# Kernel tuning notes

Hardware: AMD Instinct MI355X
Metric: run time of the kernel (lower is better)

Reference implementation:

```python
import jax, jax.numpy as jnp
import numpy as np

N_NODES = 50000
N_EDGES = 640000
DIMS = [128, 256, 128]


def setup_inputs() -> dict:
    key = jax.random.key(0)
    ks = jax.random.split(key, 8)
    x = jax.random.normal(ks[0], (N_NODES, DIMS[0]), dtype=jnp.float32)
    src = jax.random.randint(ks[1], (N_EDGES,), 0, N_NODES)
    dst = jax.random.randint(ks[2], (N_EDGES,), 0, N_NODES)
    # ensure no pre-existing self loops so add_remaining_self_loops == append all loops
    dst = jnp.where(dst == src, (dst + 1) % N_NODES, dst)
    edge_index = jnp.stack([src, dst]).astype(jnp.int64)
    # SAGEConv lin_l weights (root_weight=False -> only neighbor linear), Kaiming-ish init
    def lin(k, fan_in, fan_out):
        s = 1.0 / np.sqrt(fan_in)
        kw, kb = jax.random.split(k)
        W = jax.random.uniform(kw, (fan_out, fan_in), minval=-s, maxval=s, dtype=jnp.float32)
        b = jax.random.uniform(kb, (fan_out,), minval=-s, maxval=s, dtype=jnp.float32)
        return W, b
    W1, b1 = lin(ks[3], DIMS[0], DIMS[1])
    W2, b2 = lin(ks[4], DIMS[1], DIMS[2])
    logit_scale = jnp.asarray(np.log(1.0 / 0.07), dtype=jnp.float32)
    return {"x": x, "edge_index": edge_index, "W1": W1, "b1": b1,
            "W2": W2, "b2": b2, "logit_scale": logit_scale}


def reference(x, edge_index, W1, b1, W2, b2, logit_scale):
    N = x.shape[0]
    loops = jnp.arange(N, dtype=edge_index.dtype)
    src = jnp.concatenate([edge_index[0], loops])  # add_remaining_self_loops
    dst = jnp.concatenate([edge_index[1], loops])
    deg = jax.ops.segment_sum(jnp.ones_like(dst, dtype=x.dtype), dst, num_segments=N)
    inv_deg = 1.0 / deg  # deg >= 1 thanks to self loops

    def sage_conv(y, W, b):
        # mean aggregation of source features at destination, then linear
        agg = jax.ops.segment_sum(y[src], dst, num_segments=N) * inv_deg[:, None]
        return agg @ W.T + b

    y = jax.nn.relu(sage_conv(x, W1, b1))
    y = sage_conv(y, W2, b2)
    # F.normalize(p=2, dim=-1, eps=1e-12)
    nrm = jnp.maximum(jnp.linalg.norm(y, axis=-1, keepdims=True), 1e-12)
    y = y / nrm
    return y * jnp.exp(logit_scale)
```

## Files before the change

kernel.cpp:

```cpp
#include <hip/hip_runtime.h>
#include <hip/hip_bf16.h>

#define N_NODES 50000
#define NPAD 50048
#define ZROW N_NODES
#define D0 128
#define D1 256
#define D2 128
#define N4 1600000
#define NB4 1601536
#define CAP 128

typedef __attribute__((ext_vector_type(8))) short short8;
typedef __attribute__((ext_vector_type(8))) unsigned short ushort8;
typedef __attribute__((ext_vector_type(4))) float f32x4;

static __device__ __forceinline__ unsigned short f2bf(float f) {
    __hip_bfloat16 h = __float2bfloat16(f);
    return *(unsigned short*)&h;
}
static __device__ __forceinline__ float bf2f(unsigned short u) {
    return __uint_as_float(((unsigned int)u) << 16);
}

__global__ __launch_bounds__(256) void k_prep(const float* __restrict__ x,
                                              unsigned short* __restrict__ x_bf,
                                              int* __restrict__ cursor,
                                              const float* __restrict__ W1,
                                              const float* __restrict__ W2,
                                              unsigned short* __restrict__ W1p,
                                              unsigned short* __restrict__ W2p,
                                              const int* __restrict__ ei32,
                                              int* __restrict__ flag) {
    int idx = blockIdx.x * 256 + threadIdx.x;
    if (idx < N4) {
        float4 v = ((const float4*)x)[idx];
        ushort4 u;
        u.x = f2bf(v.x); u.y = f2bf(v.y); u.z = f2bf(v.z); u.w = f2bf(v.w);
        ((ushort4*)x_bf)[idx] = u;
    } else if (idx < NB4) {
        ushort4 z = {0, 0, 0, 0};
        ((ushort4*)x_bf)[idx] = z;
    }
    if (idx < N_NODES) cursor[idx] = 0;
    if (idx < 2 * D0 * D1) {
        if (idx < D0 * D1) {
            int j = idx & 7, lane = (idx >> 3) & 63, tile = idx >> 9;
            int ct = tile & 15, kt = tile >> 4;
            int k = kt * 32 + (lane >> 4) * 8 + j;
            int n = ct * 16 + (lane & 15);
            W1p[idx] = f2bf(W1[n * D0 + k]);
        } else {
            int i2 = idx - D0 * D1;
            int j = i2 & 7, lane = (i2 >> 3) & 63, tile = i2 >> 9;
            int ct = tile & 7, kt = tile >> 3;
            int k = kt * 32 + (lane >> 4) * 8 + j;
            int n = ct * 16 + (lane & 15);
            W2p[i2] = f2bf(W2[n * D1 + k]);
        }
    }
    if (blockIdx.x == gridDim.x - 1 && threadIdx.x < 64) {
        int lane = threadIdx.x;
        int nz = 0;
#pragma unroll
        for (int k = 0; k < 16; k++) nz += (ei32[2 * (lane * 16 + k) + 1] != 0);
#pragma unroll
        for (int off = 32; off > 0; off >>= 1) nz += __shfl_down(nz, off, 64);
        if (lane == 0) *flag = (nz == 0) ? 1 : 0;
    }
}

__global__ __launch_bounds__(256) void k_bucket(const int* __restrict__ ei,
                                                int* __restrict__ cursor,
                                                int* __restrict__ csr, int E,
                                                const int* __restrict__ flag) {
    int i = blockIdx.x * 256 + threadIdx.x;
    if (2 * i >= E) return;
    int is64 = *flag;
    int s0, d0, s1, d1;
    if (is64) {
        int4 sp = ((const int4*)ei)[i];
        int4 dp = ((const int4*)(ei + 2 * (size_t)E))[i];
        s0 = sp.x; s1 = sp.z; d0 = dp.x; d1 = dp.z;
    } else {
        int2 sp = ((const int2*)ei)[i];
        int2 dp = ((const int2*)(ei + (size_t)E))[i];
        s0 = sp.x; s1 = sp.y; d0 = dp.x; d1 = dp.y;
    }
    int p0 = atomicAdd(&cursor[d0], 1);
    if (p0 < CAP) csr[(size_t)d0 * CAP + p0] = s0;
    if (2 * i + 1 < E) {
        int p1 = atomicAdd(&cursor[d1], 1);
        if (p1 < CAP) csr[(size_t)d1 * CAP + p1] = s1;
    }
}

#define H_LD 260
__global__ __launch_bounds__(256, 4) void k_gmlp(const unsigned short* __restrict__ x_bf,
                                                 const int* __restrict__ csr,
                                                 const int* __restrict__ cursor,
                                                 const unsigned short* __restrict__ W1p,
                                                 const float* __restrict__ b1,
                                                 const unsigned short* __restrict__ W2p,
                                                 unsigned short* __restrict__ t_bf) {
    __shared__ unsigned short sbuf[4][16 * H_LD];
    int tid = threadIdx.x;
    int n0 = blockIdx.x * 64;
    int w = tid >> 6, lane = tid & 63;
    int m = lane & 15, q = lane >> 4;
    unsigned short* wbuf = sbuf[w];

    {
        int h = lane & 15;
        int sub = lane >> 4;
#pragma unroll
        for (int r = 0; r < 4; r++) {
            int lrow = r * 4 + sub;
            int node = n0 + w * 16 + lrow;
            unsigned short* lp = wbuf + lrow * H_LD + h * 8;
            if (node < N_NODES) {
                float a0[8], a1[8];
                ushort8 u = *(const ushort8*)(x_bf + (size_t)node * 128 + h * 8);
#pragma unroll
                for (int t = 0; t < 8; t++) { a0[t] = bf2f(u[t]); a1[t] = 0.f; }
                int dg = cursor[node]; if (dg > CAP) dg = CAP;
                const int* cp = csr + (size_t)node * CAP;
                int jn = (dg + 7) & ~7;
                for (int j = 0; j < jn; j += 8) {
                    int idx[8];
#pragma unroll
                    for (int u8 = 0; u8 < 8; u8++) {
                        int jj = j + u8;
                        idx[u8] = (jj < dg) ? cp[jj] : ZROW;
                    }
                    ushort8 rr[8];
#pragma unroll
                    for (int u8 = 0; u8 < 8; u8++)
                        rr[u8] = *(const ushort8*)(x_bf + (size_t)idx[u8] * 128 + h * 8);
#pragma unroll
                    for (int t = 0; t < 8; t++) {
                        a0[t] += bf2f(rr[0][t]) + bf2f(rr[2][t]) + bf2f(rr[4][t]) + bf2f(rr[6][t]);
                        a1[t] += bf2f(rr[1][t]) + bf2f(rr[3][t]) + bf2f(rr[5][t]) + bf2f(rr[7][t]);
                    }
                }
                float invd = 1.0f / (float)(dg + 1);
                ushort8 o;
#pragma unroll
                for (int t = 0; t < 8; t++) o[t] = f2bf((a0[t] + a1[t]) * invd);
                *(ushort8*)lp = o;
            } else {
                ushort8 z = {0, 0, 0, 0, 0, 0, 0, 0};
                *(ushort8*)lp = z;
            }
        }
    }

    {
        short8 af[4];
        const unsigned short* arow = wbuf + m * H_LD + q * 8;
#pragma unroll
        for (int kt = 0; kt < 4; kt++) af[kt] = *(const short8*)(arow + kt * 32);
#pragma unroll
        for (int ct = 0; ct < 16; ct++) {
            f32x4 acc = {0.f, 0.f, 0.f, 0.f};
#pragma unroll
            for (int kt = 0; kt < 4; kt++) {
                short8 bf = *(const short8*)(W1p + (((kt * 16 + ct) * 64 + lane) << 3));
                acc = __builtin_amdgcn_mfma_f32_16x16x32_bf16(af[kt], bf, acc, 0, 0, 0);
            }
            int c = ct * 16 + m;
            float bias = b1[c];
#pragma unroll
            for (int r = 0; r < 4; r++) {
                float v = fmaxf(acc[r] + bias, 0.0f);
                wbuf[(q * 4 + r) * H_LD + c] = f2bf(v);
            }
        }
    }

    {
        short8 hf[8];
        const unsigned short* hrow = wbuf + m * H_LD + q * 8;
#pragma unroll
        for (int kt = 0; kt < 8; kt++) hf[kt] = *(const short8*)(hrow + kt * 32);
#pragma unroll
        for (int ct = 0; ct < 8; ct++) {
            f32x4 acc = {0.f, 0.f, 0.f, 0.f};
#pragma unroll
            for (int kt = 0; kt < 8; kt++) {
                short8 bf = *(const short8*)(W2p + (((kt * 8 + ct) * 64 + lane) << 3));
                acc = __builtin_amdgcn_mfma_f32_16x16x32_bf16(hf[kt], bf, acc, 0, 0, 0);
            }
            int c = ct * 16 + m;
#pragma unroll
            for (int r = 0; r < 4; r++) {
                int node = n0 + w * 16 + q * 4 + r;
                t_bf[(size_t)node * 128 + c] = (node < N_NODES) ? f2bf(acc[r]) : (unsigned short)0;
            }
        }
    }
}

__global__ __launch_bounds__(256) void k_gather_final(const unsigned short* __restrict__ t,
                                                      const int* __restrict__ csr,
                                                      const int* __restrict__ cursor,
                                                      const float* __restrict__ b2,
                                                      const float* __restrict__ ls,
                                                      float* __restrict__ out) {
    int tid = threadIdx.x;
    int h = tid & 15;
    int node = blockIdx.x * 16 + (tid >> 4);

    float a0[8], a1[8];
    ushort8 u = *(const ushort8*)(t + (size_t)node * 128 + h * 8);
#pragma unroll
    for (int k = 0; k < 8; k++) { a0[k] = bf2f(u[k]); a1[k] = 0.f; }
    int dg = cursor[node]; if (dg > CAP) dg = CAP;
    const int* cp = csr + (size_t)node * CAP;
    int jn = (dg + 7) & ~7;
    for (int j = 0; j < jn; j += 8) {
        int idx[8];
#pragma unroll
        for (int u8 = 0; u8 < 8; u8++) {
            int jj = j + u8;
            idx[u8] = (jj < dg) ? cp[jj] : ZROW;
        }
        ushort8 rr[8];
#pragma unroll
        for (int u8 = 0; u8 < 8; u8++)
            rr[u8] = *(const ushort8*)(t + (size_t)idx[u8] * 128 + h * 8);
#pragma unroll
        for (int k = 0; k < 8; k++) {
            a0[k] += bf2f(rr[0][k]) + bf2f(rr[2][k]) + bf2f(rr[4][k]) + bf2f(rr[6][k]);
            a1[k] += bf2f(rr[1][k]) + bf2f(rr[3][k]) + bf2f(rr[5][k]) + bf2f(rr[7][k]);
        }
    }
    float invd = 1.0f / (float)(dg + 1);
    float4 bb0 = ((const float4*)b2)[h * 2];
    float4 bb1 = ((const float4*)b2)[h * 2 + 1];
    float v[8];
    v[0] = (a0[0] + a1[0]) * invd + bb0.x;
    v[1] = (a0[1] + a1[1]) * invd + bb0.y;
    v[2] = (a0[2] + a1[2]) * invd + bb0.z;
    v[3] = (a0[3] + a1[3]) * invd + bb0.w;
    v[4] = (a0[4] + a1[4]) * invd + bb1.x;
    v[5] = (a0[5] + a1[5]) * invd + bb1.y;
    v[6] = (a0[6] + a1[6]) * invd + bb1.z;
    v[7] = (a0[7] + a1[7]) * invd + bb1.w;

    float s = 0.f;
#pragma unroll
    for (int k = 0; k < 8; k++) s += v[k] * v[k];
#pragma unroll
    for (int msk = 8; msk > 0; msk >>= 1) s += __shfl_xor(s, msk, 64);
    float nrm = fmaxf(sqrtf(s), 1e-12f);
    float scale = expf(ls[0]) / nrm;
    float4 o0, o1;
    o0.x = v[0] * scale; o0.y = v[1] * scale; o0.z = v[2] * scale; o0.w = v[3] * scale;
    o1.x = v[4] * scale; o1.y = v[5] * scale; o1.z = v[6] * scale; o1.w = v[7] * scale;
    float* op = out + (size_t)node * 128 + h * 8;
    *(float4*)(op + 0) = o0;
    *(float4*)(op + 4) = o1;
}

extern "C" void kernel_launch(void* const* d_in, const int* in_sizes, int n_in,
                              void* d_out, int out_size, void* d_ws, size_t ws_size,
                              hipStream_t stream) {
    const float* x  = (const float*)d_in[0];
    const int*   ei = (const int*)d_in[1];
    const float* W1 = (const float*)d_in[2];
    const float* b1 = (const float*)d_in[3];
    const float* W2 = (const float*)d_in[4];
    const float* b2 = (const float*)d_in[5];
    const float* ls = (const float*)d_in[6];
    float* out = (float*)d_out;

    const int E = in_sizes[1] / 2;

    char* ws = (char*)d_ws;
    size_t off = 0;
    auto alloc = [&](size_t bytes) {
        size_t o = off;
        off = (off + bytes + 255) & ~(size_t)255;
        return o;
    };
    int*            flag   = (int*)(ws + alloc(256));
    int*            cursor = (int*)(ws + alloc((size_t)N_NODES * 4));
    int*            csr    = (int*)(ws + alloc((size_t)N_NODES * CAP * 4));
    unsigned short* W1p    = (unsigned short*)(ws + alloc((size_t)D0 * D1 * 2));
    unsigned short* W2p    = (unsigned short*)(ws + alloc((size_t)D1 * D2 * 2));
    unsigned short* x_bf   = (unsigned short*)(ws + alloc((size_t)NPAD * D0 * 2));
    unsigned short* t_bf   = (unsigned short*)(ws + alloc((size_t)NPAD * D2 * 2));

    k_prep<<<(NB4 + 255) / 256, 256, 0, stream>>>(x, x_bf, cursor, W1, W2, W1p, W2p, ei, flag);
    k_bucket<<<(E / 2 + 255) / 256, 256, 0, stream>>>(ei, cursor, csr, E, flag);
    k_gmlp<<<NPAD / 64, 256, 0, stream>>>(x_bf, csr, cursor, W1p, b1, W2p, t_bf);
    k_gather_final<<<N_NODES / 16, 256, 0, stream>>>(t_bf, csr, cursor, b2, ls, out);
}
```

Baseline: 212.6 us.

## Fuse edge bucketing into prep kernel and restructure gather-MLP work split

Merges the edge bucketing into the prep kernel. Each block re-detects the int64 index layout itself and a memset zeroes the cursor, which removes one kernel launch and the flag round trip. k_gmlp now handles 16 nodes per block: all 256 threads share the gather, then the waves split the MLP output columns, and occupancy is raised to 6. Both gathers batch the first 16 neighbor indices with vector loads so more loads are in flight. In exchange, the weight fragments are re-read by four times as many blocks, and the bucketing atomics now run in the same kernel as the conversion work.

New measurement: 200.4 us. 5.7% less time.

```diff
diff --git a/kernel.cpp b/kernel.cpp
--- a/kernel.cpp
+++ b/kernel.cpp
@@ -25,14 +25,46 @@
 
 __global__ __launch_bounds__(256) void k_prep(const float* __restrict__ x,
                                               unsigned short* __restrict__ x_bf,
-                                              int* __restrict__ cursor,
                                               const float* __restrict__ W1,
                                               const float* __restrict__ W2,
                                               unsigned short* __restrict__ W1p,
                                               unsigned short* __restrict__ W2p,
-                                              const int* __restrict__ ei32,
-                                              int* __restrict__ flag) {
+                                              const int* __restrict__ ei,
+                                              int* __restrict__ cursor,
+                                              int* __restrict__ csr, int E) {
+    __shared__ int s_is64;
+    if (threadIdx.x < 64) {
+        int lane = threadIdx.x;
+        int nz = 0;
+#pragma unroll
+        for (int k = 0; k < 16; k++) nz += (ei[2 * (lane * 16 + k) + 1] != 0);
+#pragma unroll
+        for (int off = 32; off > 0; off >>= 1) nz += __shfl_down(nz, off, 64);
+        if (lane == 0) s_is64 = (nz == 0) ? 1 : 0;
+    }
+    __syncthreads();
     int idx = blockIdx.x * 256 + threadIdx.x;
+
+    if (2 * idx < E) {
+        int is64 = s_is64;
+        int es0, ed0, es1, ed1;
+        if (is64) {
+            int4 sp = ((const int4*)ei)[idx];
+            int4 dp = ((const int4*)(ei + 2 * (size_t)E))[idx];
+            es0 = sp.x; es1 = sp.z; ed0 = dp.x; ed1 = dp.z;
+        } else {
+            int2 sp = ((const int2*)ei)[idx];
+            int2 dp = ((const int2*)(ei + (size_t)E))[idx];
+            es0 = sp.x; es1 = sp.y; ed0 = dp.x; ed1 = dp.y;
+        }
+        int p0 = atomicAdd(&cursor[ed0], 1);
+        if (p0 < CAP) csr[(size_t)ed0 * CAP + p0] = es0;
+        if (2 * idx + 1 < E) {
+            int p1 = atomicAdd(&cursor[ed1], 1);
+            if (p1 < CAP) csr[(size_t)ed1 * CAP + p1] = es1;
+        }
+    }
+
     if (idx < N4) {
         float4 v = ((const float4*)x)[idx];
         ushort4 u;
@@ -42,7 +74,7 @@
         ushort4 z = {0, 0, 0, 0};
         ((ushort4*)x_bf)[idx] = z;
     }
-    if (idx < N_NODES) cursor[idx] = 0;
+
     if (idx < 2 * D0 * D1) {
         if (idx < D0 * D1) {
             int j = idx & 7, lane = (idx >> 3) & 63, tile = idx >> 9;
@@ -59,143 +91,127 @@
             W2p[i2] = f2bf(W2[n * D1 + k]);
         }
     }
-    if (blockIdx.x == gridDim.x - 1 && threadIdx.x < 64) {
-        int lane = threadIdx.x;
-        int nz = 0;
-#pragma unroll
-        for (int k = 0; k < 16; k++) nz += (ei32[2 * (lane * 16 + k) + 1] != 0);
-#pragma unroll
-        for (int off = 32; off > 0; off >>= 1) nz += __shfl_down(nz, off, 64);
-        if (lane == 0) *flag = (nz == 0) ? 1 : 0;
-    }
-}
-
-__global__ __launch_bounds__(256) void k_bucket(const int* __restrict__ ei,
-                                                int* __restrict__ cursor,
-                                                int* __restrict__ csr, int E,
-                                                const int* __restrict__ flag) {
-    int i = blockIdx.x * 256 + threadIdx.x;
-    if (2 * i >= E) return;
-    int is64 = *flag;
-    int s0, d0, s1, d1;
-    if (is64) {
-        int4 sp = ((const int4*)ei)[i];
-        int4 dp = ((const int4*)(ei + 2 * (size_t)E))[i];
-        s0 = sp.x; s1 = sp.z; d0 = dp.x; d1 = dp.z;
-    } else {
-        int2 sp = ((const int2*)ei)[i];
-        int2 dp = ((const int2*)(ei + (size_t)E))[i];
-        s0 = sp.x; s1 = sp.y; d0 = dp.x; d1 = dp.y;
-    }
-    int p0 = atomicAdd(&cursor[d0], 1);
-    if (p0 < CAP) csr[(size_t)d0 * CAP + p0] = s0;
-    if (2 * i + 1 < E) {
-        int p1 = atomicAdd(&cursor[d1], 1);
-        if (p1 < CAP) csr[(size_t)d1 * CAP + p1] = s1;
-    }
-}
-
+}
+
+#define A_LD 132
 #define H_LD 260
-__global__ __launch_bounds__(256, 4) void k_gmlp(const unsigned short* __restrict__ x_bf,
+__global__ __launch_bounds__(256, 6) void k_gmlp(const unsigned short* __restrict__ x_bf,
                                                  const int* __restrict__ csr,
                                                  const int* __restrict__ cursor,
                                                  const unsigned short* __restrict__ W1p,
                                                  const float* __restrict__ b1,
                                                  const unsigned short* __restrict__ W2p,
                                                  unsigned short* __restrict__ t_bf) {
-    __shared__ unsigned short sbuf[4][16 * H_LD];
+    __shared__ unsigned short Abuf[16 * A_LD];
+    __shared__ unsigned short Hbuf[16 * H_LD];
     int tid = threadIdx.x;
-    int n0 = blockIdx.x * 64;
+    int n0 = blockIdx.x * 16;
+
+    {
+        int g = tid >> 4, h = tid & 15;
+        int node = n0 + g;
+        unsigned short* lp = Abuf + g * A_LD + h * 8;
+        if (node < N_NODES) {
+            int dg = cursor[node]; if (dg > CAP) dg = CAP;
+            const int* cp = csr + (size_t)node * CAP;
+            ushort8 u = *(const ushort8*)(x_bf + (size_t)node * 128 + h * 8);
+            int4 ci0 = ((const int4*)cp)[0];
+            int4 ci1 = ((const int4*)cp)[1];
+            int4 ci2 = ((const int4*)cp)[2];
+            int4 ci3 = ((const int4*)cp)[3];
+            int idx[16] = {ci0.x, ci0.y, ci0.z, ci0.w, ci1.x, ci1.y, ci1.z, ci1.w,
+                           ci2.x, ci2.y, ci2.z, ci2.w, ci3.x, ci3.y, ci3.z, ci3.w};
+#pragma unroll
+            for (int u8 = 0; u8 < 16; u8++)
+                if (u8 >= dg) idx[u8] = ZROW;
+            ushort8 rr[16];
+#pragma unroll
+            for (int u8 = 0; u8 < 16; u8++)
+                rr[u8] = *(const ushort8*)(x_bf + (size_t)idx[u8] * 128 + h * 8);
+            float a0[8], a1[8];
+#pragma unroll
+            for (int t = 0; t < 8; t++) { a0[t] = bf2f(u[t]); a1[t] = 0.f; }
+#pragma unroll
+            for (int t = 0; t < 8; t++) {
+                a0[t] += bf2f(rr[0][t]) + bf2f(rr[2][t]) + bf2f(rr[4][t]) + bf2f(rr[6][t])
+                       + bf2f(rr[8][t]) + bf2f(rr[10][t]) + bf2f(rr[12][t]) + bf2f(rr[14][t]);
+                a1[t] += bf2f(rr[1][t]) + bf2f(rr[3][t]) + bf2f(rr[5][t]) + bf2f(rr[7][t])
+                       + bf2f(rr[9][t]) + bf2f(rr[11][t]) + bf2f(rr[13][t]) + bf2f(rr[15][t]);
+            }
+            for (int j = 16; j < dg; j += 8) {
+                int idx2[8];
+#pragma unroll
+                for (int u8 = 0; u8 < 8; u8++) {
+                    int jj = j + u8;
+                    idx2[u8] = (jj < dg) ? cp[jj] : ZROW;
+                }
+                ushort8 r2[8];
+#pragma unroll
+                for (int u8 = 0; u8 < 8; u8++)
+                    r2[u8] = *(const ushort8*)(x_bf + (size_t)idx2[u8] * 128 + h * 8);
+#pragma unroll
+                for (int t = 0; t < 8; t++) {
+                    a0[t] += bf2f(r2[0][t]) + bf2f(r2[2][t]) + bf2f(r2[4][t]) + bf2f(r2[6][t]);
+                    a1[t] += bf2f(r2[1][t]) + bf2f(r2[3][t]) + bf2f(r2[5][t]) + bf2f(r2[7][t]);
+                }
+            }
+            float invd = 1.0f / (float)(dg + 1);
+            ushort8 o;
+#pragma unroll
+            for (int t = 0; t < 8; t++) o[t] = f2bf((a0[t] + a1[t]) * invd);
+            *(ushort8*)lp = o;
+        } else {
+            ushort8 z = {0, 0, 0, 0, 0, 0, 0, 0};
+            *(ushort8*)lp = z;
+        }
+    }
+    __syncthreads();
+
     int w = tid >> 6, lane = tid & 63;
     int m = lane & 15, q = lane >> 4;
-    unsigned short* wbuf = sbuf[w];
-
-    {
-        int h = lane & 15;
-        int sub = lane >> 4;
-#pragma unroll
-        for (int r = 0; r < 4; r++) {
-            int lrow = r * 4 + sub;
-            int node = n0 + w * 16 + lrow;
-            unsigned short* lp = wbuf + lrow * H_LD + h * 8;
-            if (node < N_NODES) {
-                float a0[8], a1[8];
-                ushort8 u = *(const ushort8*)(x_bf + (size_t)node * 128 + h * 8);
-#pragma unroll
-                for (int t = 0; t < 8; t++) { a0[t] = bf2f(u[t]); a1[t] = 0.f; }
-                int dg = cursor[node]; if (dg > CAP) dg = CAP;
-                const int* cp = csr + (size_t)node * CAP;
-                int jn = (dg + 7) & ~7;
-                for (int j = 0; j < jn; j += 8) {
-                    int idx[8];
-#pragma unroll
-                    for (int u8 = 0; u8 < 8; u8++) {
-                        int jj = j + u8;
-                        idx[u8] = (jj < dg) ? cp[jj] : ZROW;
-                    }
-                    ushort8 rr[8];
-#pragma unroll
-                    for (int u8 = 0; u8 < 8; u8++)
-                        rr[u8] = *(const ushort8*)(x_bf + (size_t)idx[u8] * 128 + h * 8);
-#pragma unroll
-                    for (int t = 0; t < 8; t++) {
-                        a0[t] += bf2f(rr[0][t]) + bf2f(rr[2][t]) + bf2f(rr[4][t]) + bf2f(rr[6][t]);
-                        a1[t] += bf2f(rr[1][t]) + bf2f(rr[3][t]) + bf2f(rr[5][t]) + bf2f(rr[7][t]);
-                    }
-                }
-                float invd = 1.0f / (float)(dg + 1);
-                ushort8 o;
-#pragma unroll
-                for (int t = 0; t < 8; t++) o[t] = f2bf((a0[t] + a1[t]) * invd);
-                *(ushort8*)lp = o;
-            } else {
-                ushort8 z = {0, 0, 0, 0, 0, 0, 0, 0};
-                *(ushort8*)lp = z;
-            }
-        }
-    }
 
     {
         short8 af[4];
-        const unsigned short* arow = wbuf + m * H_LD + q * 8;
+        const unsigned short* arow = Abuf + m * A_LD + q * 8;
 #pragma unroll
         for (int kt = 0; kt < 4; kt++) af[kt] = *(const short8*)(arow + kt * 32);
 #pragma unroll
-        for (int ct = 0; ct < 16; ct++) {
+        for (int c = 0; c < 4; c++) {
+            int ct = w * 4 + c;
             f32x4 acc = {0.f, 0.f, 0.f, 0.f};
 #pragma unroll
             for (int kt = 0; kt < 4; kt++) {
-                short8 bf = *(const short8*)(W1p + (((kt * 16 + ct) * 64 + lane) << 3));
-                acc = __builtin_amdgcn_mfma_f32_16x16x32_bf16(af[kt], bf, acc, 0, 0, 0);
-            }
-            int c = ct * 16 + m;
-            float bias = b1[c];
-#pragma unroll
-            for (int r = 0; r < 4; r++) {
-                float v = fmaxf(acc[r] + bias, 0.0f);
-                wbuf[(q * 4 + r) * H_LD + c] = f2bf(v);
-            }
-        }
-    }
+                short8 bw = *(const short8*)(W1p + (((kt * 16 + ct) * 64 + lane) << 3));
+                acc = __builtin_amdgcn_mfma_f32_16x16x32_bf16(af[kt], bw, acc, 0, 0, 0);
+            }
+            int col = ct * 16 + m;
+            float bias = b1[col];
+#pragma unroll
+            for (int r = 0; r < 4; r++)
+                Hbuf[(q * 4 + r) * H_LD + col] = f2bf(fmaxf(acc[r] + bias, 0.0f));
+        }
+    }
+    __syncthreads();
 
     {
         short8 hf[8];
-        const unsigned short* hrow = wbuf + m * H_LD + q * 8;
+        const unsigned short* hrow = Hbuf + m * H_LD + q * 8;
 #pragma unroll
         for (int kt = 0; kt < 8; kt++) hf[kt] = *(const short8*)(hrow + kt * 32);
 #pragma unroll
-        for (int ct = 0; ct < 8; ct++) {
+        for (int c = 0; c < 2; c++) {
+            int ct = w * 2 + c;
             f32x4 acc = {0.f, 0.f, 0.f, 0.f};
 #pragma unroll
             for (int kt = 0; kt < 8; kt++) {
-                short8 bf = *(const short8*)(W2p + (((kt * 8 + ct) * 64 + lane) << 3));
-                acc = __builtin_amdgcn_mfma_f32_16x16x32_bf16(hf[kt], bf, acc, 0, 0, 0);
-            }
-            int c = ct * 16 + m;
+                short8 bw = *(const short8*)(W2p + (((kt * 8 + ct) * 64 + lane) << 3));
+                acc = __builtin_amdgcn_mfma_f32_16x16x32_bf16(hf[kt], bw, acc, 0, 0, 0);
+            }
+            int col = ct * 16 + m;
 #pragma unroll
             for (int r = 0; r < 4; r++) {
-                int node = n0 + w * 16 + q * 4 + r;
-                t_bf[(size_t)node * 128 + c] = (node < N_NODES) ? f2bf(acc[r]) : (unsigned short)0;
+                int node = n0 + q * 4 + r;
+                t_bf[(size_t)node * 128 + col] = (node < N_NODES) ? f2bf(acc[r]) : (unsigned short)0;
             }
         }
     }
@@ -211,28 +227,47 @@
     int h = tid & 15;
     int node = blockIdx.x * 16 + (tid >> 4);
 
-    float a0[8], a1[8];
-    ushort8 u = *(const ushort8*)(t + (size_t)node * 128 + h * 8);
-#pragma unroll
-    for (int k = 0; k < 8; k++) { a0[k] = bf2f(u[k]); a1[k] = 0.f; }
     int dg = cursor[node]; if (dg > CAP) dg = CAP;
     const int* cp = csr + (size_t)node * CAP;
-    int jn = (dg + 7) & ~7;
-    for (int j = 0; j < jn; j += 8) {
-        int idx[8];
+    ushort8 u = *(const ushort8*)(t + (size_t)node * 128 + h * 8);
+    int4 ci0 = ((const int4*)cp)[0];
+    int4 ci1 = ((const int4*)cp)[1];
+    int4 ci2 = ((const int4*)cp)[2];
+    int4 ci3 = ((const int4*)cp)[3];
+    int idx[16] = {ci0.x, ci0.y, ci0.z, ci0.w, ci1.x, ci1.y, ci1.z, ci1.w,
+                   ci2.x, ci2.y, ci2.z, ci2.w, ci3.x, ci3.y, ci3.z, ci3.w};
+#pragma unroll
+    for (int u8 = 0; u8 < 16; u8++)
+        if (u8 >= dg) idx[u8] = ZROW;
+    ushort8 rr[16];
+#pragma unroll
+    for (int u8 = 0; u8 < 16; u8++)
+        rr[u8] = *(const ushort8*)(t + (size_t)idx[u8] * 128 + h * 8);
+    float a0[8], a1[8];
+#pragma unroll
+    for (int k = 0; k < 8; k++) { a0[k] = bf2f(u[k]); a1[k] = 0.f; }
+#pragma unroll
+    for (int k = 0; k < 8; k++) {
+        a0[k] += bf2f(rr[0][k]) + bf2f(rr[2][k]) + bf2f(rr[4][k]) + bf2f(rr[6][k])
+               + bf2f(rr[8][k]) + bf2f(rr[10][k]) + bf2f(rr[12][k]) + bf2f(rr[14][k]);
+        a1[k] += bf2f(rr[1][k]) + bf2f(rr[3][k]) + bf2f(rr[5][k]) + bf2f(rr[7][k])
+               + bf2f(rr[9][k]) + bf2f(rr[11][k]) + bf2f(rr[13][k]) + bf2f(rr[15][k]);
+    }
+    for (int j = 16; j < dg; j += 8) {
+        int idx2[8];
 #pragma unroll
         for (int u8 = 0; u8 < 8; u8++) {
             int jj = j + u8;
-            idx[u8] = (jj < dg) ? cp[jj] : ZROW;
-        }
-        ushort8 rr[8];
+            idx2[u8] = (jj < dg) ? cp[jj] : ZROW;
+        }
+        ushort8 r2[8];
 #pragma unroll
         for (int u8 = 0; u8 < 8; u8++)
-            rr[u8] = *(const ushort8*)(t + (size_t)idx[u8] * 128 + h * 8);
+            r2[u8] = *(const ushort8*)(t + (size_t)idx2[u8] * 128 + h * 8);
 #pragma unroll
         for (int k = 0; k < 8; k++) {
-            a0[k] += bf2f(rr[0][k]) + bf2f(rr[2][k]) + bf2f(rr[4][k]) + bf2f(rr[6][k]);
-            a1[k] += bf2f(rr[1][k]) + bf2f(rr[3][k]) + bf2f(rr[5][k]) + bf2f(rr[7][k]);
+            a0[k] += bf2f(r2[0][k]) + bf2f(r2[2][k]) + bf2f(r2[4][k]) + bf2f(r2[6][k]);
+            a1[k] += bf2f(r2[1][k]) + bf2f(r2[3][k]) + bf2f(r2[5][k]) + bf2f(r2[7][k]);
         }
     }
     float invd = 1.0f / (float)(dg + 1);
@@ -284,7 +319,6 @@
         off = (off + bytes + 255) & ~(size_t)255;
         return o;
     };
-    int*            flag   = (int*)(ws + alloc(256));
     int*            cursor = (int*)(ws + alloc((size_t)N_NODES * 4));
     int*            csr    = (int*)(ws + alloc((size_t)N_NODES * CAP * 4));
     unsigned short* W1p    = (unsigned short*)(ws + alloc((size_t)D0 * D1 * 2));
@@ -292,8 +326,8 @@
     unsigned short* x_bf   = (unsigned short*)(ws + alloc((size_t)NPAD * D0 * 2));
     unsigned short* t_bf   = (unsigned short*)(ws + alloc((size_t)NPAD * D2 * 2));
 
-    k_prep<<<(NB4 + 255) / 256, 256, 0, stream>>>(x, x_bf, cursor, W1, W2, W1p, W2p, ei, flag);
-    k_bucket<<<(E / 2 + 255) / 256, 256, 0, stream>>>(ei, cursor, csr, E, flag);
-    k_gmlp<<<NPAD / 64, 256, 0, stream>>>(x_bf, csr, cursor, W1p, b1, W2p, t_bf);
+    hipMemsetAsync(cursor, 0, (size_t)N_NODES * 4, stream);
+    k_prep<<<(NB4 + 255) / 256, 256, 0, stream>>>(x, x_bf, W1, W2, W1p, W2p, ei, cursor, csr, E);
+    k_gmlp<<<NPAD / 16, 256, 0, stream>>>(x_bf, csr, cursor, W1p, b1, W2p, t_bf);
     k_gather_final<<<N_NODES / 16, 256, 0, stream>>>(t_bf, csr, cursor, b2, ls, out);
 }
```
